# Kernel optimization log

Hardware: AMD Instinct MI355X
Metric: run time of the kernel (lower is better)

Reference implementation:

```python
import jax, jax.numpy as jnp
import numpy as np

BN_EPS = 1e-5


def conv3x3(x, w, b):
    # x: [B,C,H,W], w: [O,C,3,3], same padding, stride 1
    y = jax.lax.conv_general_dilated(x, w, (1, 1), ((1, 1), (1, 1)),
                                     dimension_numbers=('NCHW', 'OIHW', 'NCHW'))
    return y + b[None, :, None, None]


def bilinear_sample(x, py, px):
    # x: [B,C,H,W]; py/px: [B,K,H,W] fractional sample coords (zero outside borders)
    B, C, H, W = x.shape
    y0 = jnp.floor(py)
    x0 = jnp.floor(px)
    wy1 = py - y0  # frac weights
    wx1 = px - x0

    def corner(yc, xc, wgt):
        valid = (yc >= 0) & (yc <= H - 1) & (xc >= 0) & (xc <= W - 1)
        yi = jnp.clip(yc, 0, H - 1).astype(jnp.int32)
        xi = jnp.clip(xc, 0, W - 1).astype(jnp.int32)
        # gather per batch: [C,H,W] indexed by [K,H,W] -> [C,K,H,W]
        g = jax.vmap(lambda img, yy, xx: img[:, yy, xx])(x, yi, xi)  # [B,C,K,H,W]
        return g * jnp.where(valid, wgt, 0.0)[:, None]

    return (corner(y0, x0, (1 - wy1) * (1 - wx1))
            + corner(y0, x0 + 1, (1 - wy1) * wx1)
            + corner(y0 + 1, x0, wy1 * (1 - wx1))
            + corner(y0 + 1, x0 + 1, wy1 * wx1))  # [B,C,9,H,W]


def deform_conv(x, conv_w, off_w, off_b, mask_w, mask_b, gamma, beta):
    B, C, H, W = x.shape
    O = conv_w.shape[0]
    offset = conv3x3(x, off_w, off_b)                      # [B,18,H,W]
    mask = jax.nn.sigmoid(conv3x3(x, mask_w, mask_b))      # [B,9,H,W]
    off = offset.reshape(B, 9, 2, H, W)                    # tap k = kh*3+kw, (dy,dx)
    ky = jnp.repeat(jnp.arange(3), 3).astype(x.dtype)      # kernel row per tap
    kx = jnp.tile(jnp.arange(3), 3).astype(x.dtype)        # kernel col per tap
    gy = jnp.arange(H, dtype=x.dtype)
    gx = jnp.arange(W, dtype=x.dtype)
    # sample position = out pos - pad + kernel idx + learned offset
    py = off[:, :, 0] + gy[None, None, :, None] + (ky - 1.0)[None, :, None, None]
    px = off[:, :, 1] + gx[None, None, None, :] + (kx - 1.0)[None, :, None, None]
    val = bilinear_sample(x, py, px)                       # [B,C,9,H,W]
    val = val * mask[:, None]                              # modulated (DCNv2)
    out = jnp.einsum('bckhw,ock->bohw', val, conv_w.reshape(O, C, 9))
    # BatchNorm (training-mode batch stats) + ReLU
    mean = out.mean(axis=(0, 2, 3))
    var = out.var(axis=(0, 2, 3))
    out = (out - mean[None, :, None, None]) * jax.lax.rsqrt(var + BN_EPS)[None, :, None, None]
    out = out * gamma[None, :, None, None] + beta[None, :, None, None]
    return jax.nn.relu(out)


def setup_inputs() -> dict:
    key = jax.random.key(0)
    ks = jax.random.split(key, 8)
    B, Cin, Cout, H, W = 2, 64, 64, 128, 128
    x = jax.random.normal(ks[0], (B, Cin, H, W), dtype=jnp.float32)
    fan = Cin * 9
    conv_w = jax.random.normal(ks[1], (Cout, Cin, 3, 3), dtype=jnp.float32) / np.sqrt(fan)
    # offset/mask convs: small random weights so offsets are non-degenerate but modest
    off_w = jax.random.normal(ks[2], (18, Cin, 3, 3), dtype=jnp.float32) * 0.01
    off_b = jax.random.normal(ks[3], (18,), dtype=jnp.float32) * 0.1
    mask_w = jax.random.normal(ks[4], (9, Cin, 3, 3), dtype=jnp.float32) * 0.01
    mask_b = jnp.zeros((9,), dtype=jnp.float32)
    gamma = jnp.ones((Cout,), dtype=jnp.float32)
    beta = jnp.zeros((Cout,), dtype=jnp.float32)
    return {"x": x, "conv_w": conv_w, "off_w": off_w, "off_b": off_b,
            "mask_w": mask_w, "mask_b": mask_b, "gamma": gamma, "beta": beta}


def reference(x, conv_w, off_w, off_b, mask_w, mask_b, gamma, beta):
    return deform_conv(x, conv_w, off_w, off_b, mask_w, mask_b, gamma, beta)
```

## Files before the change

### kernel.cpp

```cpp
#include <hip/hip_runtime.h>
#include <hip/hip_fp16.h>

typedef __attribute__((ext_vector_type(8))) _Float16 f16x8;
typedef __attribute__((ext_vector_type(4))) float f32x4;
typedef __attribute__((ext_vector_type(4))) unsigned int u32x4;
typedef unsigned int  u32;
typedef unsigned short u16;

constexpr int B_  = 2;
constexpr int C_  = 64;
constexpr int O_  = 64;
constexpr int H_  = 128;
constexpr int W_  = 128;
constexpr int HW_ = H_ * W_;
constexpr int NPIX_ = B_ * HW_;
constexpr float BN_EPS_ = 1e-5f;

constexpr int WROWS_ = 7;
constexpr int WCOLS_ = 70;
constexpr int WPIX_  = WROWS_ * WCOLS_;
constexpr int WSTR_  = 72;

__device__ __forceinline__ u16 f2bf(float f) {
    u32 u = __float_as_uint(f);
    u = (u + 0x7fffu + ((u >> 16) & 1u)) >> 16;
    return (u16)u;
}
__device__ __forceinline__ float bflo(u32 u) { return __uint_as_float(u << 16); }
__device__ __forceinline__ float bfhi(u32 u) { return __uint_as_float(u & 0xffff0000u); }
__device__ __forceinline__ u16 f2h(float f) { return __half_as_ushort(__float2half(f)); }

__global__ __launch_bounds__(256)
void prep_kernel(const float* __restrict__ x, const float* __restrict__ conv_w,
                 const float* __restrict__ off_w, const float* __restrict__ mask_w,
                 u16* __restrict__ xt, u16* __restrict__ WpF, u16* __restrict__ W27F) {
    int bid = blockIdx.x, tid = threadIdx.x;
    if (bid < 512) {
        __shared__ u16 tile[64][66];
        int b = bid >> 8;
        int hw0 = (bid & 255) * 64;
        int c = tid >> 2, pq = (tid & 3) * 16;
        const float* src = x + (((size_t)(b * 64 + c)) << 14) + hw0 + pq;
#pragma unroll
        for (int i = 0; i < 4; i++) {
            float4 v = *(const float4*)(src + i * 4);
            tile[pq + i * 4 + 0][c] = f2h(v.x);
            tile[pq + i * 4 + 1][c] = f2h(v.y);
            tile[pq + i * 4 + 2][c] = f2h(v.z);
            tile[pq + i * 4 + 3][c] = f2h(v.w);
        }
        __syncthreads();
        int p = tid >> 2, cs = (tid & 3) * 16;
        uint4* dst = (uint4*)(xt + (((size_t)(b << 14)) + hw0 + p) * 64 + cs);
        dst[0] = *(const uint4*)&tile[p][cs];
        dst[1] = *(const uint4*)&tile[p][cs + 8];
    } else if (bid < 512 + 144) {
        int i = (bid - 512) * 256 + tid;
        int j = i & 7, lane = (i >> 3) & 63, t = (i >> 9) & 3, s = i >> 11;
        int o = t * 16 + (lane & 15);
        int kk = s * 32 + (lane >> 4) * 8 + j;
        int tap = kk >> 6, c = kk & 63;
        WpF[i] = f2h(conv_w[(o * 64 + c) * 9 + tap]);
    } else {
        int i = (bid - 656) * 256 + tid;
        int j = i & 7, lane = (i >> 3) & 63, t = (i >> 9) & 1, s = i >> 10;
        int row = t * 16 + (lane & 15);
        int kk = s * 32 + (lane >> 4) * 8 + j;
        int tap = kk >> 6, c = kk & 63;
        float v = 0.f;
        if (row < 18) v = off_w[(row * 64 + c) * 9 + tap];
        else if (row < 27) v = mask_w[((row - 18) * 64 + c) * 9 + tap];
        W27F[i] = f2h(v);
    }
}

__device__ __forceinline__ void mfma2h(const u16* __restrict__ W27F, int lane,
                                       int sg, const f16x8& sv, f32x4 (&acc)[2]) {
#pragma unroll
    for (int t = 0; t < 2; t++) {
        f16x8 af = *(const f16x8*)(W27F + (u32)((sg * 2 + t) * 64 + lane) * 8u);
        acc[t] = __builtin_amdgcn_mfma_f32_16x16x32_f16(af, sv, acc[t], 0, 0, 0);
    }
}

__device__ __forceinline__ void mfma4h(const u16* __restrict__ WpF, int lane,
                                       int sg, const f16x8& sv, f32x4 (&acc)[4]) {
#pragma unroll
    for (int t = 0; t < 4; t++) {
        f16x8 af = *(const f16x8*)(WpF + (u32)((sg * 4 + t) * 64 + lane) * 8u);
        acc[t] = __builtin_amdgcn_mfma_f32_16x16x32_f16(af, sv, acc[t], 0, 0, 0);
    }
}

__device__ __forceinline__ void metaBrt(const float* __restrict__ moff,
                                        const float* __restrict__ mmask,
                                        int tap, int p64, int h, int w, int cb,
                                        u32 qoff, u32* qc, u32* cwp) {
    float dy = moff[(2 * tap) * 64 + p64];
    float dx = moff[(2 * tap + 1) * 64 + p64];
    float m  = mmask[tap * 64 + p64];
    float kdy = (float)(tap / 3 - 1), kdx = (float)(tap % 3 - 1);
    float py = dy + (float)h + kdy;
    float px = dx + (float)w + kdx;
    float y0 = floorf(py), x0 = floorf(px);
    float ly = py - y0, lx = px - x0, hy = 1.f - ly, hx = 1.f - lx;
    float y1 = y0 + 1.f, x1 = x0 + 1.f;
    bool vy0 = (y0 >= 0.f) && (y0 <= 127.f);
    bool vy1 = (y1 >= 0.f) && (y1 <= 127.f);
    bool vx0 = (x0 >= 0.f) && (x0 <= 127.f);
    bool vx1 = (x1 >= 0.f) && (x1 <= 127.f);
    int iy0 = (int)fminf(fmaxf(y0, 0.f), 127.f);
    int iy1 = (int)fminf(fmaxf(y1, 0.f), 127.f);
    int ix0 = (int)fminf(fmaxf(x0, 0.f), 127.f);
    int ix1 = (int)fminf(fmaxf(x1, 0.f), 127.f);
    int w00 = min(max(iy0 * WCOLS_ + ix0 - cb, 0), WPIX_ - 1);
    int w01 = min(max(iy0 * WCOLS_ + ix1 - cb, 0), WPIX_ - 1);
    int w10 = min(max(iy1 * WCOLS_ + ix0 - cb, 0), WPIX_ - 1);
    int w11 = min(max(iy1 * WCOLS_ + ix1 - cb, 0), WPIX_ - 1);
    qc[0] = (u32)w00 * WSTR_ + qoff;
    qc[1] = (u32)w01 * WSTR_ + qoff;
    qc[2] = (u32)w10 * WSTR_ + qoff;
    qc[3] = (u32)w11 * WSTR_ + qoff;
    __half2 c0 = __float2half2_rn((vy0 && vx0) ? hy * hx * m : 0.f);
    __half2 c1 = __float2half2_rn((vy0 && vx1) ? hy * lx * m : 0.f);
    __half2 c2 = __float2half2_rn((vy1 && vx0) ? ly * hx * m : 0.f);
    __half2 c3 = __float2half2_rn((vy1 && vx1) ? ly * lx * m : 0.f);
    cwp[0] = *(const u32*)&c0; cwp[1] = *(const u32*)&c1;
    cwp[2] = *(const u32*)&c2; cwp[3] = *(const u32*)&c3;
}

__device__ __forceinline__ void ld4(const u16* __restrict__ win, const u32* qc,
                                    u32 sc, uint4* p) {
#pragma unroll
    for (int i = 0; i < 4; i++) p[i] = *(const uint4*)(win + qc[i] + sc);
}

__device__ __forceinline__ f16x8 cmbH(const uint4* p, const u32* cwp) {
    const u32* a = &p[0].x; const u32* b = &p[1].x;
    const u32* c = &p[2].x; const u32* d = &p[3].x;
    __half2 cw0 = *(const __half2*)&cwp[0], cw1 = *(const __half2*)&cwp[1];
    __half2 cw2 = *(const __half2*)&cwp[2], cw3 = *(const __half2*)&cwp[3];
    u32x4 r;
#pragma unroll
    for (int i = 0; i < 4; i++) {
        __half2 t = __hmul2(*(const __half2*)&a[i], cw0);
        t = __hfma2(*(const __half2*)&b[i], cw1, t);
        t = __hfma2(*(const __half2*)&c[i], cw2, t);
        t = __hfma2(*(const __half2*)&d[i], cw3, t);
        r[i] = *(const u32*)&t;
    }
    return __builtin_bit_cast(f16x8, r);
}

__global__ __launch_bounds__(256, 2)
void gemm_ab_kernel(const u16* __restrict__ xt, const u16* __restrict__ W27F,
                    const u16* __restrict__ WpF,
                    const float* __restrict__ off_b, const float* __restrict__ mask_b,
                    u16* __restrict__ pre16, float* __restrict__ part) {
    __shared__ __align__(16) u16 win[(WPIX_ + 1) * WSTR_];
    __shared__ float moff[18 * 64];
    __shared__ float mmask[9 * 64];
    const int tid = threadIdx.x;
    const int lane = tid & 63, wv = tid >> 6;
    const int quad = lane >> 4, r = lane & 15;
    const int pbase = blockIdx.x * 64;
    const int b = pbase >> 14, hwb = pbase & (HW_ - 1);
    const int h = hwb >> 7, w0 = hwb & (W_ - 1);
    const int p64 = wv * 16 + r;
    const int w = w0 + p64;
    const int cb = (h - 3) * WCOLS_ + (w0 - 3);
    const u32 bb = (u32)b << 14;
    const u32 qoff = (u32)quad * 8u;

#pragma unroll
    for (int it = 0; it < 16; it++) {
        int i = tid + it * 256;
        if (i < WPIX_ * 8) {
            int px = i >> 3, seg = i & 7;
            int wr = px / WCOLS_, wc = px - wr * WCOLS_;
            int row = min(max(h - 3 + wr, 0), H_ - 1);
            int col = min(max(w0 - 3 + wc, 0), W_ - 1);
            u32 g = (bb + (u32)(row * W_ + col)) * 64u + (u32)seg * 8u;
            *(uint4*)(&win[(u32)px * WSTR_ + (u32)seg * 8u]) = *(const uint4*)(xt + g);
        } else if (i < WPIX_ * 8 + 8) {
            int seg = i - WPIX_ * 8;
            *(uint4*)(&win[(u32)WPIX_ * WSTR_ + (u32)seg * 8u]) = make_uint4(0, 0, 0, 0);
        }
    }
    __syncthreads();

    {
        u32 aq[9];
#pragma unroll
        for (int tap = 0; tap < 9; tap++) {
            int dh = tap / 3 - 1, dw = tap % 3 - 1;
            int hh = h + dh, ww = w + dw;
            bool valid = (hh >= 0) && (hh < H_) && (ww >= 0) && (ww < W_);
            u32 widx = valid ? (u32)((3 + dh) * WCOLS_ + (p64 + 3 + dw)) : (u32)WPIX_;
            aq[tap] = widx * WSTR_ + qoff;
        }
        f32x4 accA[2];
        accA[0] = (f32x4){0.f, 0.f, 0.f, 0.f};
        accA[1] = (f32x4){0.f, 0.f, 0.f, 0.f};
        f16x8 ab[3];
        ab[0] = *(const f16x8*)(win + aq[0]);
        ab[1] = *(const f16x8*)(win + aq[0] + 32);
        ab[2] = *(const f16x8*)(win + aq[1]);
#pragma unroll
        for (int s = 0; s < 18; s++) {
            f16x8 sv = ab[s % 3];
            if (s + 3 < 18)
                ab[s % 3] = *(const f16x8*)(win + aq[(s + 3) >> 1] + ((s + 3) & 1) * 32);
            mfma2h(W27F, lane, s, sv, accA);
        }
#pragma unroll
        for (int t = 0; t < 2; t++) {
#pragma unroll
            for (int g = 0; g < 4; g++) {
                int o = t * 16 + quad * 4 + g;
                float v = accA[t][g];
                if (o < 18) {
                    moff[o * 64 + p64] = v + off_b[o];
                } else if (o < 27) {
                    v += mask_b[o - 18];
                    mmask[(o - 18) * 64 + p64] = 1.f / (1.f + __expf(-v));
                }
            }
        }
    }

    f32x4 acc[4];
#pragma unroll
    for (int t = 0; t < 4; t++) acc[t] = (f32x4){0.f, 0.f, 0.f, 0.f};

    {
        u32 q[9][4]; u32 cwv[9][4];
#pragma unroll
        for (int tap = 0; tap < 9; tap++)
            metaBrt(moff, mmask, tap, p64, h, w, cb, qoff, q[tap], cwv[tap]);

        uint4 buf[3][4];
        ld4(win, q[0], 0,  buf[0]);
        ld4(win, q[0], 32, buf[1]);
        ld4(win, q[1], 0,  buf[2]);
#pragma unroll
        for (int s = 0; s < 18; s++) {
            f16x8 sv = cmbH(buf[s % 3], cwv[s >> 1]);
            if (s + 3 < 18)
                ld4(win, q[(s + 3) >> 1], ((s + 3) & 1) * 32, buf[s % 3]);
            mfma4h(WpF, lane, s, sv, acc);
        }
    }

    const int hw = hwb + p64;
    const u32 slot = (u32)(blockIdx.x * 4 + wv);
#pragma unroll
    for (int t = 0; t < 4; t++) {
#pragma unroll
        for (int g = 0; g < 4; g++) {
            float v = acc[t][g];
            int o = t * 16 + quad * 4 + g;
            pre16[(u32)(b * 64 + o) * HW_ + hw] = f2bf(v);
            float s = v, s2 = v * v;
#pragma unroll
            for (int off = 8; off >= 1; off >>= 1) {
                s  += __shfl_down(s, off, 16);
                s2 += __shfl_down(s2, off, 16);
            }
            if (r == 0) {
                part[(u32)o * 2048 + slot] = s;
                part[131072 + (u32)o * 2048 + slot] = s2;
            }
        }
    }
}

__global__ __launch_bounds__(256)
void stats_red_kernel(const float* __restrict__ part, float* __restrict__ stats) {
    __shared__ float p4[4];
    int i = blockIdx.x;
    const float* src = part + (u32)(i >> 6) * 131072 + (u32)(i & 63) * 2048;
    float s = 0.f;
    for (int rr = threadIdx.x; rr < 2048; rr += 256) s += src[rr];
#pragma unroll
    for (int off = 32; off >= 1; off >>= 1) s += __shfl_down(s, off);
    if ((threadIdx.x & 63) == 0) p4[threadIdx.x >> 6] = s;
    __syncthreads();
    if (threadIdx.x == 0) stats[i] = p4[0] + p4[1] + p4[2] + p4[3];
}

__global__ __launch_bounds__(256)
void bn_relu_kernel(const u16* __restrict__ pre16, const float* __restrict__ stats,
                    const float* __restrict__ gamma, const float* __restrict__ beta,
                    float* __restrict__ out) {
    int i4 = blockIdx.x * 256 + threadIdx.x;
    int ch = (i4 >> 12) & (O_ - 1);
    float mean = stats[ch] * (1.f / NPIX_);
    float var  = stats[64 + ch] * (1.f / NPIX_) - mean * mean;
    float scale = gamma[ch] * rsqrtf(var + BN_EPS_);
    float shift = beta[ch] - mean * scale;
    uint2 v = ((const uint2*)pre16)[i4];
    float4 o;
    o.x = fmaxf(fmaf(bflo(v.x), scale, shift), 0.f);
    o.y = fmaxf(fmaf(bfhi(v.x), scale, shift), 0.f);
    o.z = fmaxf(fmaf(bflo(v.y), scale, shift), 0.f);
    o.w = fmaxf(fmaf(bfhi(v.y), scale, shift), 0.f);
    ((float4*)out)[i4] = o;
}

extern "C" void kernel_launch(void* const* d_in, const int* in_sizes, int n_in,
                              void* d_out, int out_size, void* d_ws, size_t ws_size,
                              hipStream_t stream) {
    const float* x      = (const float*)d_in[0];
    const float* conv_w = (const float*)d_in[1];
    const float* off_w  = (const float*)d_in[2];
    const float* off_b  = (const float*)d_in[3];
    const float* mask_w = (const float*)d_in[4];
    const float* mask_b = (const float*)d_in[5];
    const float* gamma  = (const float*)d_in[6];
    const float* beta   = (const float*)d_in[7];
    float* out = (float*)d_out;

    char* ws = (char*)d_ws;
    u16*  xt     = (u16*)(ws);
    u16*  pre16  = (u16*)(ws + 4194432);
    u16*  WpF    = (u16*)(ws + 8388736);
    u16*  W27F   = (u16*)(ws + 8462464);
    float* part  = (float*)(ws + 8499328);
    float* stats = (float*)(ws + 9547904);

    prep_kernel<<<728, 256, 0, stream>>>(x, conv_w, off_w, mask_w, xt, WpF, W27F);
    gemm_ab_kernel<<<NPIX_ / 64, 256, 0, stream>>>(xt, W27F, WpF, off_b, mask_b, pre16, part);
    stats_red_kernel<<<128, 256, 0, stream>>>(part, stats);
    bn_relu_kernel<<<2048, 256, 0, stream>>>(pre16, stats, gamma, beta, out);
}
```

Before: 100.5 us.

## Split gemm block into two wave groups sharing K and reducing via LDS

The main gemm kernel now runs 512 threads (8 waves) per 64-pixel block instead of 256. For the offset/mask conv each wave group computes one of the two 16-row output tiles. For the deformable conv the 18 K-steps are split in half across the two groups, and the partial accumulators are summed through shared memory before the stores and statistics. This doubles the waves available to hide LDS and MFMA latency and halves per-thread register arrays, at the cost of extra barriers, an LDS reduction, and some duplicated metadata computation (tap 4 is computed by both groups).

Measured after the change: 108.9 us. 1.08x slower.

```diff
diff --git a/kernel.cpp b/kernel.cpp
--- a/kernel.cpp
+++ b/kernel.cpp
@@ -71,15 +71,6 @@
         if (row < 18) v = off_w[(row * 64 + c) * 9 + tap];
         else if (row < 27) v = mask_w[((row - 18) * 64 + c) * 9 + tap];
         W27F[i] = f2h(v);
-    }
-}
-
-__device__ __forceinline__ void mfma2h(const u16* __restrict__ W27F, int lane,
-                                       int sg, const f16x8& sv, f32x4 (&acc)[2]) {
-#pragma unroll
-    for (int t = 0; t < 2; t++) {
-        f16x8 af = *(const f16x8*)(W27F + (u32)((sg * 2 + t) * 64 + lane) * 8u);
-        acc[t] = __builtin_amdgcn_mfma_f32_16x16x32_f16(af, sv, acc[t], 0, 0, 0);
     }
 }
 
@@ -152,7 +143,7 @@
     return __builtin_bit_cast(f16x8, r);
 }
 
-__global__ __launch_bounds__(256, 2)
+__global__ __launch_bounds__(512, 4)
 void gemm_ab_kernel(const u16* __restrict__ xt, const u16* __restrict__ W27F,
                     const u16* __restrict__ WpF,
                     const float* __restrict__ off_b, const float* __restrict__ mask_b,
@@ -163,18 +154,19 @@
     const int tid = threadIdx.x;
     const int lane = tid & 63, wv = tid >> 6;
     const int quad = lane >> 4, r = lane & 15;
+    const int wp = wv & 3, os = wv >> 2;
     const int pbase = blockIdx.x * 64;
     const int b = pbase >> 14, hwb = pbase & (HW_ - 1);
     const int h = hwb >> 7, w0 = hwb & (W_ - 1);
-    const int p64 = wv * 16 + r;
+    const int p64 = wp * 16 + r;
     const int w = w0 + p64;
     const int cb = (h - 3) * WCOLS_ + (w0 - 3);
     const u32 bb = (u32)b << 14;
     const u32 qoff = (u32)quad * 8u;
 
 #pragma unroll
-    for (int it = 0; it < 16; it++) {
-        int i = tid + it * 256;
+    for (int it = 0; it < 8; it++) {
+        int i = tid + it * 512;
         if (i < WPIX_ * 8) {
             int px = i >> 3, seg = i & 7;
             int wr = px / WCOLS_, wc = px - wr * WCOLS_;
@@ -199,9 +191,7 @@
             u32 widx = valid ? (u32)((3 + dh) * WCOLS_ + (p64 + 3 + dw)) : (u32)WPIX_;
             aq[tap] = widx * WSTR_ + qoff;
         }
-        f32x4 accA[2];
-        accA[0] = (f32x4){0.f, 0.f, 0.f, 0.f};
-        accA[1] = (f32x4){0.f, 0.f, 0.f, 0.f};
+        f32x4 accA = (f32x4){0.f, 0.f, 0.f, 0.f};
         f16x8 ab[3];
         ab[0] = *(const f16x8*)(win + aq[0]);
         ab[1] = *(const f16x8*)(win + aq[0] + 32);
@@ -211,65 +201,83 @@
             f16x8 sv = ab[s % 3];
             if (s + 3 < 18)
                 ab[s % 3] = *(const f16x8*)(win + aq[(s + 3) >> 1] + ((s + 3) & 1) * 32);
-            mfma2h(W27F, lane, s, sv, accA);
-        }
-#pragma unroll
-        for (int t = 0; t < 2; t++) {
+            f16x8 af = *(const f16x8*)(W27F + (u32)((s * 2 + os) * 64 + lane) * 8u);
+            accA = __builtin_amdgcn_mfma_f32_16x16x32_f16(af, sv, accA, 0, 0, 0);
+        }
+#pragma unroll
+        for (int g = 0; g < 4; g++) {
+            int o = os * 16 + quad * 4 + g;
+            float v = accA[g];
+            if (o < 18) {
+                moff[o * 64 + p64] = v + off_b[o];
+            } else if (o < 27) {
+                v += mask_b[o - 18];
+                mmask[(o - 18) * 64 + p64] = 1.f / (1.f + __expf(-v));
+            }
+        }
+    }
+    __syncthreads();
+
+    f32x4 acc[4];
+#pragma unroll
+    for (int t = 0; t < 4; t++) acc[t] = (f32x4){0.f, 0.f, 0.f, 0.f};
+
+    {
+        const int tb = os * 4;
+        const int s0 = os * 9;
+        u32 q[5][4]; u32 cwv[5][4];
+#pragma unroll
+        for (int lt = 0; lt < 5; lt++)
+            metaBrt(moff, mmask, tb + lt, p64, h, w, cb, qoff, q[lt], cwv[lt]);
+
+        uint4 buf[2][4];
+        ld4(win, q[0], (u32)((s0 & 1) * 32), buf[0]);
+#pragma unroll
+        for (int ls = 0; ls < 9; ls++) {
+            int s = s0 + ls;
+            f16x8 sv = cmbH(buf[ls & 1], cwv[(s >> 1) - tb]);
+            if (ls < 8) {
+                int s2 = s + 1;
+                ld4(win, q[(s2 >> 1) - tb], (u32)((s2 & 1) * 32), buf[(ls + 1) & 1]);
+            }
+            mfma4h(WpF, lane, s, sv, acc);
+        }
+    }
+    __syncthreads();
+
+    float* ex = (float*)win;
+    const u32 exi = (u32)(wp * 16 + r) * 68u + (u32)quad * 4u;
+    if (os == 1) {
+#pragma unroll
+        for (int t = 0; t < 4; t++)
+            *(f32x4*)(ex + exi + (u32)t * 16u) = acc[t];
+    }
+    __syncthreads();
+
+    if (os == 0) {
+#pragma unroll
+        for (int t = 0; t < 4; t++)
+            acc[t] += *(const f32x4*)(ex + exi + (u32)t * 16u);
+
+        const int hw = hwb + p64;
+        const u32 slot = (u32)(blockIdx.x * 4 + wp);
+#pragma unroll
+        for (int t = 0; t < 4; t++) {
 #pragma unroll
             for (int g = 0; g < 4; g++) {
+                float v = acc[t][g];
                 int o = t * 16 + quad * 4 + g;
-                float v = accA[t][g];
-                if (o < 18) {
-                    moff[o * 64 + p64] = v + off_b[o];
-                } else if (o < 27) {
-                    v += mask_b[o - 18];
-                    mmask[(o - 18) * 64 + p64] = 1.f / (1.f + __expf(-v));
+                pre16[(u32)(b * 64 + o) * HW_ + hw] = f2bf(v);
+                float s = v, s2 = v * v;
+#pragma unroll
+                for (int off = 8; off >= 1; off >>= 1) {
+                    s  += __shfl_down(s, off, 16);
+                    s2 += __shfl_down(s2, off, 16);
                 }
-            }
-        }
-    }
-
-    f32x4 acc[4];
-#pragma unroll
-    for (int t = 0; t < 4; t++) acc[t] = (f32x4){0.f, 0.f, 0.f, 0.f};
-
-    {
-        u32 q[9][4]; u32 cwv[9][4];
-#pragma unroll
-        for (int tap = 0; tap < 9; tap++)
-            metaBrt(moff, mmask, tap, p64, h, w, cb, qoff, q[tap], cwv[tap]);
-
-        uint4 buf[3][4];
-        ld4(win, q[0], 0,  buf[0]);
-        ld4(win, q[0], 32, buf[1]);
-        ld4(win, q[1], 0,  buf[2]);
-#pragma unroll
-        for (int s = 0; s < 18; s++) {
-            f16x8 sv = cmbH(buf[s % 3], cwv[s >> 1]);
-            if (s + 3 < 18)
-                ld4(win, q[(s + 3) >> 1], ((s + 3) & 1) * 32, buf[s % 3]);
-            mfma4h(WpF, lane, s, sv, acc);
-        }
-    }
-
-    const int hw = hwb + p64;
-    const u32 slot = (u32)(blockIdx.x * 4 + wv);
-#pragma unroll
-    for (int t = 0; t < 4; t++) {
-#pragma unroll
-        for (int g = 0; g < 4; g++) {
-            float v = acc[t][g];
-            int o = t * 16 + quad * 4 + g;
-            pre16[(u32)(b * 64 + o) * HW_ + hw] = f2bf(v);
-            float s = v, s2 = v * v;
-#pragma unroll
-            for (int off = 8; off >= 1; off >>= 1) {
-                s  += __shfl_down(s, off, 16);
-                s2 += __shfl_down(s2, off, 16);
-            }
-            if (r == 0) {
-                part[(u32)o * 2048 + slot] = s;
-                part[131072 + (u32)o * 2048 + slot] = s2;
+                if (r == 0) {
+                    part[(u32)o * 2048 + slot] = s;
+                    part[131072 + (u32)o * 2048 + slot] = s2;
+                }
             }
         }
     }
@@ -330,7 +338,7 @@
     float* stats = (float*)(ws + 9547904);
 
     prep_kernel<<<728, 256, 0, stream>>>(x, conv_w, off_w, mask_w, xt, WpF, W27F);
-    gemm_ab_kernel<<<NPIX_ / 64, 256, 0, stream>>>(xt, W27F, WpF, off_b, mask_b, pre16, part);
+    gemm_ab_kernel<<<NPIX_ / 64, 512, 0, stream>>>(xt, W27F, WpF, off_b, mask_b, pre16, part);
     stats_red_kernel<<<128, 256, 0, stream>>>(part, stats);
     bn_relu_kernel<<<2048, 256, 0, stream>>>(pre16, stats, gamma, beta, out);
 }
```
